# Kernel optimization log

Measured on AMD Instinct MI355X. Metric: run time of the kernel, lower is better.

## Reference

```python
import jax, jax.numpy as jnp
import numpy as np

B, NV, NH, D = 16, 1024, 1024, 1024
NEG = -1e30


def setup_inputs() -> dict:
    key = jax.random.key(0)
    ks = jax.random.split(key, 12)
    sc = 1.0 / np.sqrt(D)
    return {
        "v": jax.random.normal(ks[0], (B, NV, D), jnp.float32),
        "h": jax.random.normal(ks[1], (B, NH, D), jnp.float32),
        "z": jax.random.normal(ks[2], (B, NV, 2 * D), jnp.float32),
        "v_mask": jnp.ones((B, NV), jnp.int32),
        "h_mask": jnp.ones((B, NH), jnp.int32),
        # learned parameters (torch Linear convention: W [out,in])
        "Wv_w": jax.random.normal(ks[3], (D, D), jnp.float32) * sc,
        "Wv_b": jax.random.normal(ks[4], (D,), jnp.float32) * sc,
        "Wh_w": jax.random.normal(ks[5], (D, D), jnp.float32) * sc,
        "qv_w": jax.random.normal(ks[6], (D, D), jnp.float32) * sc,
        "qv_b": jax.random.normal(ks[7], (D,), jnp.float32) * sc,
        "kh_w": jax.random.normal(ks[8], (D, D), jnp.float32) * sc,
        "Wz_w": jax.random.normal(ks[9], (D, 2 * D), jnp.float32) * sc,
        "Wu_w": jax.random.normal(ks[10], (1, D), jnp.float32) * sc,
    }


def reference(v, h, z, v_mask, h_mask, Wv_w, Wv_b, Wh_w, qv_w, qv_b, kh_w, Wz_w, Wu_w):
    v_v = v @ Wv_w.T + Wv_b                    # [B,NV,D]
    h_h = h @ Wh_w.T                           # [B,NH,D]
    z_z = z @ Wz_w.T                           # [B,NV,D]
    query = v @ qv_w.T + qv_b                  # [B,NV,D]
    key = h @ kh_w.T                           # [B,NH,D]
    key = jnp.where(h_mask[:, :, None] == 0, NEG, key)
    att = jnp.einsum('bqd,bkd->bqk', query, key)       # [B,NV,NH]
    h_v = jnp.einsum('bqk,bkd->bqd', jax.nn.softmax(att, axis=-1), h_h)
    s = jax.nn.sigmoid(v_v + h_v + z_z)        # [B,NV,D]
    # W_u(s_i + s_j) == u_i + u_j since W_u is linear with no bias
    u = jnp.einsum('bnd,d->bn', s, Wu_w[0])    # [B,NV]
    f = u[:, :, None] + u[:, None, :]          # [B,NV,NV] pairwise scores
    f = jnp.where(v_mask[:, None, :] == 0, NEG, f)
    f = jnp.einsum('bij,bjd->bid', jax.nn.softmax(f, axis=-1), v)  # [B,NV,D]
    h_new = f
    z_new = jnp.concatenate((s, f), axis=-1)   # [B,NV,2D]
    return h_new, z_new
```

## Files before the change

### kernel.cpp

```cpp
#include <hip/hip_runtime.h>

#define BB 16
#define NV 1024
#define NH 1024
#define DD 1024

typedef _Float16 f16x8 __attribute__((ext_vector_type(8)));
typedef _Float16 f16x4 __attribute__((ext_vector_type(4)));
typedef float f32x4 __attribute__((ext_vector_type(4)));

__global__ __launch_bounds__(256) void cast_k(const float* __restrict__ in,
                                              _Float16* __restrict__ out, long n4) {
  long i = (long)blockIdx.x * 256 + threadIdx.x;
  long stride = (long)gridDim.x * 256;
  for (; i < n4; i += stride) {
    float4 x = ((const float4*)in)[i];
    f16x4 o;
    o[0] = (_Float16)x.x; o[1] = (_Float16)x.y;
    o[2] = (_Float16)x.z; o[3] = (_Float16)x.w;
    ((f16x4*)out)[i] = o;
  }
}

__global__ __launch_bounds__(256) void split_k(const float* __restrict__ in,
                                               _Float16* __restrict__ hi,
                                               _Float16* __restrict__ lo, long n4) {
  long i = (long)blockIdx.x * 256 + threadIdx.x;
  long stride = (long)gridDim.x * 256;
  for (; i < n4; i += stride) {
    float4 x = ((const float4*)in)[i];
    f16x4 h, l;
    h[0] = (_Float16)x.x; h[1] = (_Float16)x.y;
    h[2] = (_Float16)x.z; h[3] = (_Float16)x.w;
    l[0] = (_Float16)(x.x - (float)h[0]);
    l[1] = (_Float16)(x.y - (float)h[1]);
    l[2] = (_Float16)(x.z - (float)h[2]);
    l[3] = (_Float16)(x.w - (float)h[3]);
    ((f16x4*)hi)[i] = h;
    ((f16x4*)lo)[i] = l;
  }
}

__device__ inline void gl_lds16(const _Float16* g, _Float16* l) {
  __builtin_amdgcn_global_load_lds((__attribute__((address_space(1))) void*)g,
                                   (__attribute__((address_space(3))) void*)l,
                                   16, 0, 0);
}

__device__ inline void decode_tiles(int flat, int NB, int& bm, int& bn, int& bz) {
  int xcd = flat & 7, j = flat >> 3;
  if (NB == 1) {
    bz = 0;
    bm = xcd * 16 + (j >> 3);
    bn = j & 7;
  } else {
    bz = xcd * 2 + (j >> 6);
    int r = j & 63;
    bm = r >> 3;
    bn = r & 7;
  }
}

template <typename CT>
__global__ __launch_bounds__(256) void gemm_nt_k(
    const _Float16* __restrict__ A, const _Float16* __restrict__ B,
    CT* __restrict__ C, const float* __restrict__ bias,
    int K, int NB, long sA, long sB, long sC) {
  __shared__ _Float16 lA[128 * 32];
  __shared__ _Float16 lB[128 * 32];
  const int tid = threadIdx.x;
  const int w = tid >> 6, l = tid & 63;
  int bm, bn, bz;
  decode_tiles(blockIdx.x, NB, bm, bn, bz);
  const _Float16* Ab = A + (long)bz * sA;
  const _Float16* Bb = B + (long)bz * sB;
  CT* Cb = C + (long)bz * sC;

  const int c0 = 2 * w;
  const int srow = l >> 2, scol = (l & 3) * 8;
  const _Float16* pA = Ab + (long)(bm * 128 + c0 * 16 + srow) * K + scol;
  const _Float16* pB = Bb + (long)(bn * 128 + c0 * 16 + srow) * K + scol;
  const long rs16 = (long)16 * K;
  _Float16* dA = lA + c0 * 16 * 32;
  _Float16* dB = lB + c0 * 16 * 32;

  f32x4 acc[4][4] = {};
  const int wm = w >> 1, wn = w & 1;
  const int fr = l & 15, fq = l >> 4;
  const int aoff = (wm * 64 + fr) * 32 + fq * 8;
  const int boff = (wn * 64 + fr) * 32 + fq * 8;

  for (int kt = 0; kt < K; kt += 32) {
    gl_lds16(pA, dA);
    gl_lds16(pA + rs16, dA + 512);
    gl_lds16(pB, dB);
    gl_lds16(pB + rs16, dB + 512);
    pA += 32; pB += 32;
    __syncthreads();
    f16x8 af[4], bf[4];
#pragma unroll
    for (int r = 0; r < 4; ++r) af[r] = *(const f16x8*)&lA[aoff + r * 512];
#pragma unroll
    for (int c = 0; c < 4; ++c) bf[c] = *(const f16x8*)&lB[boff + c * 512];
#pragma unroll
    for (int r = 0; r < 4; ++r)
#pragma unroll
      for (int c = 0; c < 4; ++c)
        acc[r][c] = __builtin_amdgcn_mfma_f32_16x16x32_f16(af[r], bf[c], acc[r][c], 0, 0, 0);
    __syncthreads();
  }

#pragma unroll
  for (int r = 0; r < 4; ++r) {
    const int grow = bm * 128 + wm * 64 + r * 16 + fq * 4;
#pragma unroll
    for (int c = 0; c < 4; ++c) {
      const int gcol = bn * 128 + wn * 64 + c * 16 + fr;
      const float bv = bias ? bias[gcol] : 0.0f;
#pragma unroll
      for (int e = 0; e < 4; ++e)
        Cb[(long)(grow + e) * 1024 + gcol] = (CT)(acc[r][c][e] + bv);
    }
  }
}

template <bool SPLIT_OUT>
__global__ __launch_bounds__(256) void gemm3_nt_k(
    const _Float16* __restrict__ Ahi, const _Float16* __restrict__ Alo,
    const _Float16* __restrict__ Bhi, const _Float16* __restrict__ Blo,
    float* __restrict__ Cf, _Float16* __restrict__ Chi, _Float16* __restrict__ Clo,
    const float* __restrict__ bias, const int* __restrict__ mask,
    int K, int NB, long sA, long sB, long sC) {
  __shared__ _Float16 lAh[128 * 32];
  __shared__ _Float16 lAl[128 * 32];
  __shared__ _Float16 lBh[128 * 32];
  __shared__ _Float16 lBl[128 * 32];
  const int tid = threadIdx.x;
  const int w = tid >> 6, l = tid & 63;
  int bm, bn, bz;
  decode_tiles(blockIdx.x, NB, bm, bn, bz);

  const int c0 = 2 * w;
  const int srow = l >> 2, scol = (l & 3) * 8;
  const long arow = (long)(bm * 128 + c0 * 16 + srow) * K + scol + (long)bz * sA;
  const long brow = (long)(bn * 128 + c0 * 16 + srow) * K + scol + (long)bz * sB;
  const _Float16* pAh = Ahi + arow;
  const _Float16* pAl = Alo + arow;
  const _Float16* pBh = Bhi + brow;
  const _Float16* pBl = Blo + brow;
  const long rs16 = (long)16 * K;
  const int dofs = c0 * 512;

  f32x4 acc[4][4] = {};
  const int wm = w >> 1, wn = w & 1;
  const int fr = l & 15, fq = l >> 4;
  const int aoff = (wm * 64 + fr) * 32 + fq * 8;
  const int boff = (wn * 64 + fr) * 32 + fq * 8;

  for (int kt = 0; kt < K; kt += 32) {
    gl_lds16(pAh, lAh + dofs);
    gl_lds16(pAh + rs16, lAh + dofs + 512);
    gl_lds16(pAl, lAl + dofs);
    gl_lds16(pAl + rs16, lAl + dofs + 512);
    gl_lds16(pBh, lBh + dofs);
    gl_lds16(pBh + rs16, lBh + dofs + 512);
    gl_lds16(pBl, lBl + dofs);
    gl_lds16(pBl + rs16, lBl + dofs + 512);
    pAh += 32; pAl += 32; pBh += 32; pBl += 32;
    __syncthreads();
    f16x8 ah[4], al[4], bh[4], bl[4];
#pragma unroll
    for (int r = 0; r < 4; ++r) {
      ah[r] = *(const f16x8*)&lAh[aoff + r * 512];
      al[r] = *(const f16x8*)&lAl[aoff + r * 512];
    }
#pragma unroll
    for (int c = 0; c < 4; ++c) {
      bh[c] = *(const f16x8*)&lBh[boff + c * 512];
      bl[c] = *(const f16x8*)&lBl[boff + c * 512];
    }
#pragma unroll
    for (int r = 0; r < 4; ++r)
#pragma unroll
      for (int c = 0; c < 4; ++c) {
        acc[r][c] = __builtin_amdgcn_mfma_f32_16x16x32_f16(ah[r], bh[c], acc[r][c], 0, 0, 0);
        acc[r][c] = __builtin_amdgcn_mfma_f32_16x16x32_f16(al[r], bh[c], acc[r][c], 0, 0, 0);
        acc[r][c] = __builtin_amdgcn_mfma_f32_16x16x32_f16(ah[r], bl[c], acc[r][c], 0, 0, 0);
      }
    __syncthreads();
  }

#pragma unroll
  for (int r = 0; r < 4; ++r) {
    const int grow = bm * 128 + wm * 64 + r * 16 + fq * 4;
#pragma unroll
    for (int c = 0; c < 4; ++c) {
      const int gcol = bn * 128 + wn * 64 + c * 16 + fr;
      const float bv = bias ? bias[gcol] : 0.0f;
#pragma unroll
      for (int e = 0; e < 4; ++e) {
        float val = acc[r][c][e] + bv;
        if (mask && mask[grow + e] == 0) val = -30000.0f;
        const long idx = (long)(grow + e) * 1024 + gcol + (long)bz * sC;
        if (SPLIT_OUT) {
          _Float16 hi = (_Float16)val;
          Chi[idx] = hi;
          Clo[idx] = (_Float16)(val - (float)hi);
        } else {
          Cf[idx] = val;
        }
      }
    }
  }
}

__device__ inline float wave_max(float v) {
#pragma unroll
  for (int o = 32; o > 0; o >>= 1) v = fmaxf(v, __shfl_xor(v, o, 64));
  return v;
}
__device__ inline float wave_sum(float v) {
#pragma unroll
  for (int o = 32; o > 0; o >>= 1) v += __shfl_xor(v, o, 64);
  return v;
}

__global__ __launch_bounds__(256) void softmax_rows_k(const float* __restrict__ att,
                                                      _Float16* __restrict__ P) {
  __shared__ float red[4];
  long row = blockIdx.x;
  int t = threadIdx.x, w = t >> 6;
  float4 x = ((const float4*)(att + row * 1024))[t];
  float m = fmaxf(fmaxf(x.x, x.y), fmaxf(x.z, x.w));
  m = wave_max(m);
  if ((t & 63) == 0) red[w] = m;
  __syncthreads();
  m = fmaxf(fmaxf(red[0], red[1]), fmaxf(red[2], red[3]));
  float e0 = expf(x.x - m), e1 = expf(x.y - m), e2 = expf(x.z - m), e3 = expf(x.w - m);
  float s = wave_sum(e0 + e1 + e2 + e3);
  __syncthreads();
  if ((t & 63) == 0) red[w] = s;
  __syncthreads();
  float inv = 1.0f / (red[0] + red[1] + red[2] + red[3]);
  f16x4 o;
  o[0] = (_Float16)(e0 * inv); o[1] = (_Float16)(e1 * inv);
  o[2] = (_Float16)(e2 * inv); o[3] = (_Float16)(e3 * inv);
  ((f16x4*)(P + row * 1024))[t] = o;
}

__global__ __launch_bounds__(256) void s_u_k(const _Float16* __restrict__ Vv,
                                             const float* __restrict__ Hv,
                                             const _Float16* __restrict__ Zz,
                                             const float* __restrict__ Wu,
                                             float* __restrict__ zout,
                                             float* __restrict__ u) {
  __shared__ float red[4];
  long row = blockIdx.x;
  int t = threadIdx.x, w = t >> 6;
  f16x4 a = ((const f16x4*)(Vv + row * 1024))[t];
  float4 b = ((const float4*)(Hv + row * 1024))[t];
  f16x4 c = ((const f16x4*)(Zz + row * 1024))[t];
  float4 wu = ((const float4*)Wu)[t];
  float4 sv;
  sv.x = 1.0f / (1.0f + expf(-((float)a[0] + b.x + (float)c[0])));
  sv.y = 1.0f / (1.0f + expf(-((float)a[1] + b.y + (float)c[1])));
  sv.z = 1.0f / (1.0f + expf(-((float)a[2] + b.z + (float)c[2])));
  sv.w = 1.0f / (1.0f + expf(-((float)a[3] + b.w + (float)c[3])));
  ((float4*)(zout + row * 2048))[t] = sv;
  float part = sv.x * wu.x + sv.y * wu.y + sv.z * wu.z + sv.w * wu.w;
  part = wave_sum(part);
  if ((t & 63) == 0) red[w] = part;
  __syncthreads();
  if (t == 0) u[row] = red[0] + red[1] + red[2] + red[3];
}

__global__ __launch_bounds__(256) void u_softmax_k(const float* __restrict__ u,
                                                   const int* __restrict__ vmask,
                                                   float* __restrict__ p) {
  __shared__ float red[4];
  int b = blockIdx.x, t = threadIdx.x, w = t >> 6;
  float4 uv = ((const float4*)(u + b * 1024))[t];
  int4 mv = ((const int4*)(vmask + b * 1024))[t];
  float l0 = mv.x ? uv.x : -1e30f;
  float l1 = mv.y ? uv.y : -1e30f;
  float l2 = mv.z ? uv.z : -1e30f;
  float l3 = mv.w ? uv.w : -1e30f;
  float m = wave_max(fmaxf(fmaxf(l0, l1), fmaxf(l2, l3)));
  if ((t & 63) == 0) red[w] = m;
  __syncthreads();
  m = fmaxf(fmaxf(red[0], red[1]), fmaxf(red[2], red[3]));
  float e0 = expf(l0 - m), e1 = expf(l1 - m), e2 = expf(l2 - m), e3 = expf(l3 - m);
  float s = wave_sum(e0 + e1 + e2 + e3);
  __syncthreads();
  if ((t & 63) == 0) red[w] = s;
  __syncthreads();
  float inv = 1.0f / (red[0] + red[1] + red[2] + red[3]);
  float4 o = make_float4(e0 * inv, e1 * inv, e2 * inv, e3 * inv);
  ((float4*)(p + b * 1024))[t] = o;
}

__global__ __launch_bounds__(256) void f_part_k(const float* __restrict__ p,
                                               const float* __restrict__ v,
                                               float* __restrict__ f) {
  int d = blockIdx.x * 256 + threadIdx.x;
  int b = blockIdx.y;
  int jc = blockIdx.z;
  const float* vb = v + ((long)b * NV + jc * 128) * DD + d;
  const float* pb = p + b * NV + jc * 128;
  float acc = 0.0f;
#pragma unroll 4
  for (int j = 0; j < 128; ++j) acc = fmaf(pb[j], vb[(long)j * DD], acc);
  atomicAdd(&f[b * DD + d], acc);
}

__global__ __launch_bounds__(256) void bcast_k(const float* __restrict__ f,
                                               float* __restrict__ hout,
                                               float* __restrict__ zout) {
  long idx = (long)blockIdx.x * 256 + threadIdx.x;
  int d4 = (int)(idx & 255);
  long bn = idx >> 8;
  int b = (int)(bn >> 10);
  float4 val = ((const float4*)f)[(b << 8) + d4];
  ((float4*)hout)[idx] = val;
  ((float4*)zout)[bn * 512 + 256 + d4] = val;
}

extern "C" void kernel_launch(void* const* d_in, const int* in_sizes, int n_in,
                              void* d_out, int out_size, void* d_ws, size_t ws_size,
                              hipStream_t stream) {
  const float* v = (const float*)d_in[0];
  const float* h = (const float*)d_in[1];
  const float* z = (const float*)d_in[2];
  const int* v_mask = (const int*)d_in[3];
  const int* h_mask = (const int*)d_in[4];
  const float* Wv_w = (const float*)d_in[5];
  const float* Wv_b = (const float*)d_in[6];
  const float* Wh_w = (const float*)d_in[7];
  const float* qv_w = (const float*)d_in[8];
  const float* qv_b = (const float*)d_in[9];
  const float* kh_w = (const float*)d_in[10];
  const float* Wz_w = (const float*)d_in[11];
  const float* Wu_w = (const float*)d_in[12];

  float* h_new = (float*)d_out;
  float* z_new = (float*)d_out + (long)BB * NV * DD;

  const size_t MB = 1u << 20;
  char* W = (char*)d_ws;
  _Float16* vhi  = (_Float16*)(W + 0 * MB);
  _Float16* vlo  = (_Float16*)(W + 32 * MB);
  _Float16* P16  = (_Float16*)(W + 32 * MB);
  _Float16* hhi  = (_Float16*)(W + 64 * MB);
  _Float16* hlo  = (_Float16*)(W + 96 * MB);
  _Float16* Hht16 = (_Float16*)(W + 96 * MB);
  _Float16* z16  = (_Float16*)(W + 128 * MB);
  _Float16* qvhi = (_Float16*)(W + 192 * MB);
  _Float16* qvlo = (_Float16*)(W + 194 * MB);
  _Float16* khhi = (_Float16*)(W + 196 * MB);
  _Float16* khlo = (_Float16*)(W + 198 * MB);
  _Float16* Wv16 = (_Float16*)(W + 200 * MB);
  _Float16* Wh16 = (_Float16*)(W + 202 * MB);
  _Float16* Wz16 = (_Float16*)(W + 204 * MB);
  _Float16* Qhi  = (_Float16*)(W + 208 * MB);
  _Float16* Vv16 = (_Float16*)(W + 208 * MB);
  _Float16* Qlo  = (_Float16*)(W + 240 * MB);
  _Float16* Zz16 = (_Float16*)(W + 240 * MB);
  _Float16* Khi  = (_Float16*)(W + 272 * MB);
  _Float16* Klo  = (_Float16*)(W + 304 * MB);
  float*    Hv32 = (float*)(W + 272 * MB);
  float*    att32 = (float*)(W + 336 * MB);
  float*    u_buf = (float*)(W + 400 * MB);
  float*    p_buf = (float*)(W + 400 * MB + 65536);
  float*    f_buf = (float*)(W + 400 * MB + 2 * 65536);

  const long nVD = (long)BB * NV * DD;
  const long s1M = (long)NV * DD;

  auto cast = [&](const float* src, _Float16* dst, long n) {
    long n4 = n / 4;
    cast_k<<<(int)((n4 + 255) / 256), 256, 0, stream>>>(src, dst, n4);
  };
  auto split = [&](const float* src, _Float16* hi, _Float16* lo, long n) {
    long n4 = n / 4;
    split_k<<<(int)((n4 + 255) / 256), 256, 0, stream>>>(src, hi, lo, n4);
  };

  split(v, vhi, vlo, nVD);
  split(h, hhi, hlo, nVD);
  cast(z, z16, nVD * 2);
  split(qv_w, qvhi, qvlo, (long)DD * DD);
  split(kh_w, khhi, khlo, (long)DD * DD);
  cast(Wv_w, Wv16, (long)DD * DD);
  cast(Wh_w, Wh16, (long)DD * DD);
  cast(Wz_w, Wz16, (long)DD * 2 * DD);

  gemm3_nt_k<true><<<1024, 256, 0, stream>>>(vhi, vlo, qvhi, qvlo,
      nullptr, Qhi, Qlo, qv_b, nullptr, DD, 1, 0, 0, 0);
  gemm3_nt_k<true><<<1024, 256, 0, stream>>>(hhi, hlo, khhi, khlo,
      nullptr, Khi, Klo, nullptr, h_mask, DD, 1, 0, 0, 0);
  gemm3_nt_k<false><<<1024, 256, 0, stream>>>(Qhi, Qlo, Khi, Klo,
      att32, nullptr, nullptr, nullptr, nullptr, DD, BB, s1M, s1M, s1M);
  softmax_rows_k<<<BB * NV, 256, 0, stream>>>(att32, P16);
  gemm_nt_k<_Float16><<<1024, 256, 0, stream>>>(Wh16, hhi, Hht16, nullptr, DD, BB, 0, s1M, s1M);
  gemm_nt_k<_Float16><<<1024, 256, 0, stream>>>(vhi, Wv16, Vv16, Wv_b, DD, 1, 0, 0, 0);
  gemm_nt_k<_Float16><<<1024, 256, 0, stream>>>(z16, Wz16, Zz16, nullptr, 2 * DD, 1, 0, 0, 0);
  gemm_nt_k<float><<<1024, 256, 0, stream>>>(P16, Hht16, Hv32, nullptr, NH, BB, s1M, s1M, s1M);
  s_u_k<<<BB * NV, 256, 0, stream>>>(Vv16, Hv32, Zz16, Wu_w, z_new, u_buf);
  u_softmax_k<<<BB, 256, 0, stream>>>(u_buf, v_mask, p_buf);
  hipMemsetAsync(f_buf, 0, (long)BB * DD * 4, stream);
  f_part_k<<<dim3(4, BB, 8), 256, 0, stream>>>(p_buf, v, f_buf);
  bcast_k<<<(int)(nVD / 4 / 256), 256, 0, stream>>>(f_buf, h_new, z_new);
}
```

Baseline: 1.204 ms.

## Switch GEMMs to 256x256 tiles with multi-stage async LDS pipelining

Replaces the 128x128 single-buffered GEMM kernels with 256x256-tile, 512-thread kernels. The plain GEMM uses a 4-deep LDS ring with 3 stages in flight, and the split-precision GEMM uses double buffering. Both wait on explicit vmcnt and raise MFMA priority with setprio. The goal is to hide global-load latency behind matrix math and to cut global and LDS traffic per FLOP through larger tiles. In exchange each block uses 128KB of LDS and many more accumulator registers. The grid drops to 256 blocks, which may leave some CUs idle on a 256-CU part.

```diff
diff --git a/kernel.cpp b/kernel.cpp
--- a/kernel.cpp
+++ b/kernel.cpp
@@ -47,159 +47,224 @@
                                    16, 0, 0);
 }
 
-__device__ inline void decode_tiles(int flat, int NB, int& bm, int& bn, int& bz) {
+__device__ inline void decode256(int flat, int NB, int& bm, int& bn, int& bz) {
   int xcd = flat & 7, j = flat >> 3;
   if (NB == 1) {
     bz = 0;
-    bm = xcd * 16 + (j >> 3);
-    bn = j & 7;
+    bm = xcd * 8 + (j >> 2);
+    bn = j & 3;
   } else {
-    bz = xcd * 2 + (j >> 6);
-    int r = j & 63;
-    bm = r >> 3;
-    bn = r & 7;
+    bz = xcd * 2 + (j >> 4);
+    int r = j & 15;
+    bm = r >> 2;
+    bn = r & 3;
   }
 }
 
 template <typename CT>
-__global__ __launch_bounds__(256) void gemm_nt_k(
+__global__ __launch_bounds__(512) void gemm256_nt_k(
     const _Float16* __restrict__ A, const _Float16* __restrict__ B,
     CT* __restrict__ C, const float* __restrict__ bias,
     int K, int NB, long sA, long sB, long sC) {
-  __shared__ _Float16 lA[128 * 32];
-  __shared__ _Float16 lB[128 * 32];
+  __shared__ _Float16 lds[65536];
   const int tid = threadIdx.x;
   const int w = tid >> 6, l = tid & 63;
   int bm, bn, bz;
-  decode_tiles(blockIdx.x, NB, bm, bn, bz);
+  decode256(blockIdx.x, NB, bm, bn, bz);
   const _Float16* Ab = A + (long)bz * sA;
   const _Float16* Bb = B + (long)bz * sB;
   CT* Cb = C + (long)bz * sC;
 
-  const int c0 = 2 * w;
-  const int srow = l >> 2, scol = (l & 3) * 8;
-  const _Float16* pA = Ab + (long)(bm * 128 + c0 * 16 + srow) * K + scol;
-  const _Float16* pB = Bb + (long)(bn * 128 + c0 * 16 + srow) * K + scol;
-  const long rs16 = (long)16 * K;
-  _Float16* dA = lA + c0 * 16 * 32;
-  _Float16* dB = lB + c0 * 16 * 32;
-
-  f32x4 acc[4][4] = {};
-  const int wm = w >> 1, wn = w & 1;
+  const int srow = w * 16 + (l >> 2);
+  const int sslot = l & 3;
+  const _Float16* gA = Ab + (long)(bm * 256 + srow) * K + sslot * 8;
+  const _Float16* gB = Bb + (long)(bn * 256 + srow) * K + sslot * 8;
+  const long rs128 = (long)128 * K;
+  const int T = K >> 5;
+
   const int fr = l & 15, fq = l >> 4;
-  const int aoff = (wm * 64 + fr) * 32 + fq * 8;
+  const int wm = w >> 2, wn = w & 3;
+  const int aoff = (wm * 128 + fr) * 32 + fq * 8;
   const int boff = (wn * 64 + fr) * 32 + fq * 8;
 
-  for (int kt = 0; kt < K; kt += 32) {
+  f32x4 acc[8][4] = {};
+
+  auto stage = [&](int st) {
+    _Float16* dA = lds + (st & 3) * 16384 + w * 512;
+    _Float16* dB = dA + 8192;
+    const _Float16* pA = gA + st * 32;
+    const _Float16* pB = gB + st * 32;
     gl_lds16(pA, dA);
-    gl_lds16(pA + rs16, dA + 512);
+    gl_lds16(pA + rs128, dA + 4096);
     gl_lds16(pB, dB);
-    gl_lds16(pB + rs16, dB + 512);
-    pA += 32; pB += 32;
-    __syncthreads();
-    f16x8 af[4], bf[4];
-#pragma unroll
-    for (int r = 0; r < 4; ++r) af[r] = *(const f16x8*)&lA[aoff + r * 512];
-#pragma unroll
-    for (int c = 0; c < 4; ++c) bf[c] = *(const f16x8*)&lB[boff + c * 512];
-#pragma unroll
-    for (int r = 0; r < 4; ++r)
-#pragma unroll
-      for (int c = 0; c < 4; ++c)
-        acc[r][c] = __builtin_amdgcn_mfma_f32_16x16x32_f16(af[r], bf[c], acc[r][c], 0, 0, 0);
-    __syncthreads();
-  }
-
-#pragma unroll
-  for (int r = 0; r < 4; ++r) {
-    const int grow = bm * 128 + wm * 64 + r * 16 + fq * 4;
-#pragma unroll
-    for (int c = 0; c < 4; ++c) {
-      const int gcol = bn * 128 + wn * 64 + c * 16 + fr;
+    gl_lds16(pB + rs128, dB + 4096);
+  };
+
+  stage(0); stage(1); stage(2);
+  asm volatile("s_waitcnt vmcnt(8)" ::: "memory");
+  __builtin_amdgcn_s_barrier();
+  __builtin_amdgcn_sched_barrier(0);
+
+  for (int t = 0; t < T; ++t) {
+    const _Float16* bufA = lds + (t & 3) * 16384;
+    const _Float16* bufB = bufA + 8192;
+    if (t + 3 < T) stage(t + 3);
+    f16x8 bf[4], af[4];
+#pragma unroll
+    for (int n = 0; n < 4; ++n) bf[n] = *(const f16x8*)&bufB[boff + n * 512];
+#pragma unroll
+    for (int m = 0; m < 4; ++m) af[m] = *(const f16x8*)&bufA[aoff + m * 512];
+    __builtin_amdgcn_s_setprio(1);
+#pragma unroll
+    for (int m = 0; m < 4; ++m)
+#pragma unroll
+      for (int n = 0; n < 4; ++n)
+        acc[m][n] = __builtin_amdgcn_mfma_f32_16x16x32_f16(af[m], bf[n], acc[m][n], 0, 0, 0);
+    __builtin_amdgcn_s_setprio(0);
+#pragma unroll
+    for (int m = 0; m < 4; ++m) af[m] = *(const f16x8*)&bufA[aoff + (m + 4) * 512];
+    __builtin_amdgcn_s_setprio(1);
+#pragma unroll
+    for (int m = 0; m < 4; ++m)
+#pragma unroll
+      for (int n = 0; n < 4; ++n)
+        acc[m + 4][n] = __builtin_amdgcn_mfma_f32_16x16x32_f16(af[m], bf[n], acc[m + 4][n], 0, 0, 0);
+    __builtin_amdgcn_s_setprio(0);
+    if (t + 1 < T) {
+      const int hi = (t + 3 < T) ? t + 3 : T - 1;
+      const int cnt = 4 * (hi - (t + 1));
+      if (cnt >= 8)      asm volatile("s_waitcnt vmcnt(8)" ::: "memory");
+      else if (cnt == 4) asm volatile("s_waitcnt vmcnt(4)" ::: "memory");
+      else               asm volatile("s_waitcnt vmcnt(0)" ::: "memory");
+      __builtin_amdgcn_s_barrier();
+      __builtin_amdgcn_sched_barrier(0);
+    }
+  }
+
+#pragma unroll
+  for (int m = 0; m < 8; ++m) {
+    const int grow = bm * 256 + wm * 128 + m * 16 + fq * 4;
+#pragma unroll
+    for (int n = 0; n < 4; ++n) {
+      const int gcol = bn * 256 + wn * 64 + n * 16 + fr;
       const float bv = bias ? bias[gcol] : 0.0f;
 #pragma unroll
       for (int e = 0; e < 4; ++e)
-        Cb[(long)(grow + e) * 1024 + gcol] = (CT)(acc[r][c][e] + bv);
+        Cb[(long)(grow + e) * 1024 + gcol] = (CT)(acc[m][n][e] + bv);
     }
   }
 }
 
 template <bool SPLIT_OUT>
-__global__ __launch_bounds__(256) void gemm3_nt_k(
+__global__ __launch_bounds__(512) void gemm3_256_k(
     const _Float16* __restrict__ Ahi, const _Float16* __restrict__ Alo,
     const _Float16* __restrict__ Bhi, const _Float16* __restrict__ Blo,
     float* __restrict__ Cf, _Float16* __restrict__ Chi, _Float16* __restrict__ Clo,
     const float* __restrict__ bias, const int* __restrict__ mask,
     int K, int NB, long sA, long sB, long sC) {
-  __shared__ _Float16 lAh[128 * 32];
-  __shared__ _Float16 lAl[128 * 32];
-  __shared__ _Float16 lBh[128 * 32];
-  __shared__ _Float16 lBl[128 * 32];
+  __shared__ _Float16 lds[65536];
   const int tid = threadIdx.x;
   const int w = tid >> 6, l = tid & 63;
   int bm, bn, bz;
-  decode_tiles(blockIdx.x, NB, bm, bn, bz);
-
-  const int c0 = 2 * w;
-  const int srow = l >> 2, scol = (l & 3) * 8;
-  const long arow = (long)(bm * 128 + c0 * 16 + srow) * K + scol + (long)bz * sA;
-  const long brow = (long)(bn * 128 + c0 * 16 + srow) * K + scol + (long)bz * sB;
-  const _Float16* pAh = Ahi + arow;
-  const _Float16* pAl = Alo + arow;
-  const _Float16* pBh = Bhi + brow;
-  const _Float16* pBl = Blo + brow;
-  const long rs16 = (long)16 * K;
-  const int dofs = c0 * 512;
-
-  f32x4 acc[4][4] = {};
-  const int wm = w >> 1, wn = w & 1;
+  decode256(blockIdx.x, NB, bm, bn, bz);
+
+  const int srow = w * 16 + (l >> 2);
+  const int sslot = l & 3;
+  const long abase = (long)(bm * 256 + srow) * K + sslot * 8 + (long)bz * sA;
+  const long bbase = (long)(bn * 256 + srow) * K + sslot * 8 + (long)bz * sB;
+  const _Float16* gAh = Ahi + abase;
+  const _Float16* gAl = Alo + abase;
+  const _Float16* gBh = Bhi + bbase;
+  const _Float16* gBl = Blo + bbase;
+  const long rs128 = (long)128 * K;
+  const int T = K >> 5;
+
   const int fr = l & 15, fq = l >> 4;
-  const int aoff = (wm * 64 + fr) * 32 + fq * 8;
+  const int wm = w >> 2, wn = w & 3;
+  const int aoff = (wm * 128 + fr) * 32 + fq * 8;
   const int boff = (wn * 64 + fr) * 32 + fq * 8;
 
-  for (int kt = 0; kt < K; kt += 32) {
-    gl_lds16(pAh, lAh + dofs);
-    gl_lds16(pAh + rs16, lAh + dofs + 512);
-    gl_lds16(pAl, lAl + dofs);
-    gl_lds16(pAl + rs16, lAl + dofs + 512);
-    gl_lds16(pBh, lBh + dofs);
-    gl_lds16(pBh + rs16, lBh + dofs + 512);
-    gl_lds16(pBl, lBl + dofs);
-    gl_lds16(pBl + rs16, lBl + dofs + 512);
-    pAh += 32; pAl += 32; pBh += 32; pBl += 32;
-    __syncthreads();
-    f16x8 ah[4], al[4], bh[4], bl[4];
-#pragma unroll
-    for (int r = 0; r < 4; ++r) {
-      ah[r] = *(const f16x8*)&lAh[aoff + r * 512];
-      al[r] = *(const f16x8*)&lAl[aoff + r * 512];
-    }
-#pragma unroll
-    for (int c = 0; c < 4; ++c) {
-      bh[c] = *(const f16x8*)&lBh[boff + c * 512];
-      bl[c] = *(const f16x8*)&lBl[boff + c * 512];
-    }
-#pragma unroll
-    for (int r = 0; r < 4; ++r)
-#pragma unroll
-      for (int c = 0; c < 4; ++c) {
-        acc[r][c] = __builtin_amdgcn_mfma_f32_16x16x32_f16(ah[r], bh[c], acc[r][c], 0, 0, 0);
-        acc[r][c] = __builtin_amdgcn_mfma_f32_16x16x32_f16(al[r], bh[c], acc[r][c], 0, 0, 0);
-        acc[r][c] = __builtin_amdgcn_mfma_f32_16x16x32_f16(ah[r], bl[c], acc[r][c], 0, 0, 0);
+  f32x4 acc[8][4] = {};
+
+  auto stage = [&](int st) {
+    _Float16* d = lds + (st & 1) * 32768 + w * 512;
+    const int ko = st * 32;
+    gl_lds16(gAh + ko, d);
+    gl_lds16(gAh + ko + rs128, d + 4096);
+    gl_lds16(gAl + ko, d + 8192);
+    gl_lds16(gAl + ko + rs128, d + 12288);
+    gl_lds16(gBh + ko, d + 16384);
+    gl_lds16(gBh + ko + rs128, d + 20480);
+    gl_lds16(gBl + ko, d + 24576);
+    gl_lds16(gBl + ko + rs128, d + 28672);
+  };
+
+  stage(0); stage(1);
+  asm volatile("s_waitcnt vmcnt(8)" ::: "memory");
+  __builtin_amdgcn_s_barrier();
+  __builtin_amdgcn_sched_barrier(0);
+
+  for (int t = 0; t < T; ++t) {
+    const _Float16* bA = lds + (t & 1) * 32768;
+    const _Float16* bB = bA + 16384;
+    f16x8 bh[4], bl[4], ah[4], al[4];
+#pragma unroll
+    for (int n = 0; n < 4; ++n) {
+      bh[n] = *(const f16x8*)&bB[boff + n * 512];
+      bl[n] = *(const f16x8*)&bB[8192 + boff + n * 512];
+    }
+#pragma unroll
+    for (int m = 0; m < 4; ++m) {
+      ah[m] = *(const f16x8*)&bA[aoff + m * 512];
+      al[m] = *(const f16x8*)&bA[8192 + aoff + m * 512];
+    }
+    __builtin_amdgcn_s_setprio(1);
+#pragma unroll
+    for (int m = 0; m < 4; ++m)
+#pragma unroll
+      for (int n = 0; n < 4; ++n) {
+        acc[m][n] = __builtin_amdgcn_mfma_f32_16x16x32_f16(ah[m], bh[n], acc[m][n], 0, 0, 0);
+        acc[m][n] = __builtin_amdgcn_mfma_f32_16x16x32_f16(al[m], bh[n], acc[m][n], 0, 0, 0);
+        acc[m][n] = __builtin_amdgcn_mfma_f32_16x16x32_f16(ah[m], bl[n], acc[m][n], 0, 0, 0);
       }
-    __syncthreads();
-  }
-
-#pragma unroll
-  for (int r = 0; r < 4; ++r) {
-    const int grow = bm * 128 + wm * 64 + r * 16 + fq * 4;
-#pragma unroll
-    for (int c = 0; c < 4; ++c) {
-      const int gcol = bn * 128 + wn * 64 + c * 16 + fr;
+    __builtin_amdgcn_s_setprio(0);
+#pragma unroll
+    for (int m = 0; m < 4; ++m) {
+      ah[m] = *(const f16x8*)&bA[aoff + (m + 4) * 512];
+      al[m] = *(const f16x8*)&bA[8192 + aoff + (m + 4) * 512];
+    }
+    asm volatile("s_waitcnt lgkmcnt(0)" ::: "memory");
+    __builtin_amdgcn_s_barrier();
+    __builtin_amdgcn_sched_barrier(0);
+    if (t + 2 < T) stage(t + 2);
+    __builtin_amdgcn_s_setprio(1);
+#pragma unroll
+    for (int m = 0; m < 4; ++m)
+#pragma unroll
+      for (int n = 0; n < 4; ++n) {
+        acc[m + 4][n] = __builtin_amdgcn_mfma_f32_16x16x32_f16(ah[m], bh[n], acc[m + 4][n], 0, 0, 0);
+        acc[m + 4][n] = __builtin_amdgcn_mfma_f32_16x16x32_f16(al[m], bh[n], acc[m + 4][n], 0, 0, 0);
+        acc[m + 4][n] = __builtin_amdgcn_mfma_f32_16x16x32_f16(ah[m], bl[n], acc[m + 4][n], 0, 0, 0);
+      }
+    __builtin_amdgcn_s_setprio(0);
+    if (t + 1 < T) {
+      if (t + 2 < T) asm volatile("s_waitcnt vmcnt(8)" ::: "memory");
+      else           asm volatile("s_waitcnt vmcnt(0)" ::: "memory");
+      __builtin_amdgcn_s_barrier();
+      __builtin_amdgcn_sched_barrier(0);
+    }
+  }
+
+#pragma unroll
+  for (int m = 0; m < 8; ++m) {
+    const int grow = bm * 256 + wm * 128 + m * 16 + fq * 4;
+#pragma unroll
+    for (int n = 0; n < 4; ++n) {
+      const int gcol = bn * 256 + wn * 64 + n * 16 + fr;
       const float bv = bias ? bias[gcol] : 0.0f;
 #pragma unroll
       for (int e = 0; e < 4; ++e) {
-        float val = acc[r][c][e] + bv;
+        float val = acc[m][n][e] + bv;
         if (mask && mask[grow + e] == 0) val = -30000.0f;
         const long idx = (long)(grow + e) * 1024 + gcol + (long)bz * sC;
         if (SPLIT_OUT) {
@@ -394,17 +459,17 @@
   cast(Wh_w, Wh16, (long)DD * DD);
   cast(Wz_w, Wz16, (long)DD * 2 * DD);
 
-  gemm3_nt_k<true><<<1024, 256, 0, stream>>>(vhi, vlo, qvhi, qvlo,
+  gemm3_256_k<true><<<256, 512, 0, stream>>>(vhi, vlo, qvhi, qvlo,
       nullptr, Qhi, Qlo, qv_b, nullptr, DD, 1, 0, 0, 0);
-  gemm3_nt_k<true><<<1024, 256, 0, stream>>>(hhi, hlo, khhi, khlo,
+  gemm3_256_k<true><<<256, 512, 0, stream>>>(hhi, hlo, khhi, khlo,
       nullptr, Khi, Klo, nullptr, h_mask, DD, 1, 0, 0, 0);
-  gemm3_nt_k<false><<<1024, 256, 0, stream>>>(Qhi, Qlo, Khi, Klo,
+  gemm3_256_k<false><<<256, 512, 0, stream>>>(Qhi, Qlo, Khi, Klo,
       att32, nullptr, nullptr, nullptr, nullptr, DD, BB, s1M, s1M, s1M);
   softmax_rows_k<<<BB * NV, 256, 0, stream>>>(att32, P16);
-  gemm_nt_k<_Float16><<<1024, 256, 0, stream>>>(Wh16, hhi, Hht16, nullptr, DD, BB, 0, s1M, s1M);
-  gemm_nt_k<_Float16><<<1024, 256, 0, stream>>>(vhi, Wv16, Vv16, Wv_b, DD, 1, 0, 0, 0);
-  gemm_nt_k<_Float16><<<1024, 256, 0, stream>>>(z16, Wz16, Zz16, nullptr, 2 * DD, 1, 0, 0, 0);
-  gemm_nt_k<float><<<1024, 256, 0, stream>>>(P16, Hht16, Hv32, nullptr, NH, BB, s1M, s1M, s1M);
+  gemm256_nt_k<_Float16><<<256, 512, 0, stream>>>(Wh16, hhi, Hht16, nullptr, DD, BB, 0, s1M, s1M);
+  gemm256_nt_k<_Float16><<<256, 512, 0, stream>>>(vhi, Wv16, Vv16, Wv_b, DD, 1, 0, 0, 0);
+  gemm256_nt_k<_Float16><<<256, 512, 0, stream>>>(z16, Wz16, Zz16, nullptr, 2 * DD, 1, 0, 0, 0);
+  gemm256_nt_k<float><<<256, 512, 0, stream>>>(P16, Hht16, Hv32, nullptr, NH, BB, s1M, s1M, s1M);
   s_u_k<<<BB * NV, 256, 0, stream>>>(Vv16, Hv32, Zz16, Wu_w, z_new, u_buf);
   u_softmax_k<<<BB, 256, 0, stream>>>(u_buf, v_mask, p_buf);
   hipMemsetAsync(f_buf, 0, (long)BB * DD * 4, stream);
```

Measured after the change: 1.023 ms. -15.1%, faster.
